# Kernel tuning notes

Hardware: AMD Instinct MI355X
Metric: run time of the kernel (lower is better)

The kernel has to match this reference:

```python
import jax, jax.numpy as jnp
import numpy as np

BN_EPS = 1e-5

def _conv(x, w, b, pad):
    # x: [B,C,H,W], w: [O,I,kh,kw] -> [B,O,H,W]
    y = jax.lax.conv_general_dilated(x, w, window_strides=(1, 1),
                                     padding=[(pad, pad), (pad, pad)],
                                     dimension_numbers=("NCHW", "OIHW", "NCHW"))
    return y + b[None, :, None, None]

def setup_inputs() -> dict:
    key = jax.random.key(0)
    ks = jax.random.split(key, 5)
    B, Cin, H, W = 2, 256, 80, 80
    Ck, Cv, Cout = 128, 256, 256
    std = 0.02  # matches torch normal_(0, 0.02) init
    return {
        "x": jax.random.normal(ks[0], (B, Cin, H, W), jnp.float32),
        "wk": std * jax.random.normal(ks[1], (Ck, Cin, 1, 1), jnp.float32),
        "bk": jnp.zeros((Ck,), jnp.float32),
        "gamma": jnp.ones((Ck,), jnp.float32),
        "beta": jnp.zeros((Ck,), jnp.float32),
        "rmean": jnp.zeros((Ck,), jnp.float32),
        "rvar": jnp.ones((Ck,), jnp.float32),
        "wv": std * jax.random.normal(ks[2], (Cv, Cin, 3, 3), jnp.float32),
        "bv": jnp.zeros((Cv,), jnp.float32),
        "ww": std * jax.random.normal(ks[3], (Cout, Cv, 1, 1), jnp.float32),
        "bw": jnp.zeros((Cout,), jnp.float32),
    }

def reference(x, wk, bk, gamma, beta, rmean, rvar, wv, bv, ww, bw):
    B, Cin, H, W = x.shape
    Ck, Cv = wk.shape[0], wv.shape[0]
    N = H * W

    # f_key == f_query (shared module): 1x1 conv + BatchNorm (inference stats)
    kq = _conv(x, wk, bk, pad=0)                      # [B,Ck,H,W]
    inv = gamma / jnp.sqrt(rvar + BN_EPS)
    kq = kq * inv[None, :, None, None] + (beta - rmean * inv)[None, :, None, None]
    kq = kq.reshape(B, Ck, N)                          # key layout [B,Ck,N]

    # f_value: 3x3 conv
    value = _conv(x, wv, bv, pad=1).reshape(B, Cv, N)  # [B,Cv,N]

    # sim_map = query^T @ key -> [B,N,N], full softmax over last dim
    sim = jnp.einsum("bcn,bcm->bnm", kq, kq)
    sim = jax.nn.softmax(sim, axis=-1)

    # context = sim @ value^T -> [B,N,Cv] -> [B,Cv,H,W]
    ctx = jnp.einsum("bnm,bcm->bcn", sim, value).reshape(B, Cv, H, W)

    out = _conv(ctx, ww, bw, pad=0) + x                # residual
    return out
```

## Files before the change

### kernel.cpp

```cpp
#include <hip/hip_runtime.h>
#include <math.h>

#define NB   2
#define CIN  256
#define IMH  80
#define IMW  80
#define NPIX (IMH*IMW)
#define CK   128
#define CVC  256
#define COUTC 256
#define BN_EPS 1e-5f
#define HP   82
#define WP   82
#define SPLIT 2
#define NC   (NPIX / SPLIT / 64)
#define NMC  (NPIX / 64)

typedef short sx8 __attribute__((ext_vector_type(8)));
typedef short sx4 __attribute__((ext_vector_type(4)));
typedef float f32x4 __attribute__((ext_vector_type(4)));

__device__ __forceinline__ short f2bf(float f) {
    unsigned u = __builtin_bit_cast(unsigned, f);
    u += 0x7fffu + ((u >> 16) & 1u);
    return (short)(u >> 16);
}
__device__ __forceinline__ float bf2f(short s) {
    unsigned u = ((unsigned)(unsigned short)s) << 16;
    return __builtin_bit_cast(float, u);
}

__global__ __launch_bounds__(256) void pad_kernel(const float* __restrict__ x,
                                                  short* __restrict__ xpad)
{
    __shared__ short T[64][258];
    const int tid = threadIdx.x;
    const int n0  = blockIdx.x * 64;
    const int b   = blockIdx.y;
    const float* xb = x + (size_t)b * CIN * NPIX;

    #pragma unroll 4
    for (int i = 0; i < 64; ++i) {
        int e = tid + i * 256;
        int pix = e & 63, c = e >> 6;
        T[pix][c] = f2bf(xb[(size_t)c * NPIX + n0 + pix]);
    }
    __syncthreads();
    #pragma unroll
    for (int i = 0; i < 8; ++i) {
        int e   = tid + i * 256;
        int pix = e >> 5;
        int cp  = (e & 31) * 8;
        int np  = n0 + pix;
        int hp  = np / IMW + 1, wp = np % IMW + 1;
        sx8 v = *(const sx8*)&T[pix][cp];
        *(sx8*)&xpad[(((size_t)b * HP + hp) * WP + wp) * CIN + cp] = v;
    }
}

__global__ __launch_bounds__(256) void wvt_kernel(const float* __restrict__ wv,
                                                  short* __restrict__ wvt)
{
    int idx = blockIdx.x * 256 + threadIdx.x;
    int tap = idx >> 16;
    int cv  = (idx >> 8) & 255;
    int c   = idx & 255;
    wvt[idx] = f2bf(wv[((size_t)cv * CIN + c) * 9 + tap]);
}

__global__ __launch_bounds__(256) void wwb_kernel(const float* __restrict__ ww,
                                                  short* __restrict__ wwb)
{
    int idx = blockIdx.x * 256 + threadIdx.x;
    wwb[idx] = f2bf(ww[idx]);
}

__global__ __launch_bounds__(256) void wkb_kernel(
    const float* __restrict__ wk, const float* __restrict__ bk,
    const float* __restrict__ gamma, const float* __restrict__ beta,
    const float* __restrict__ rmean, const float* __restrict__ rvar,
    short* __restrict__ wkb, float* __restrict__ bias2)
{
    int idx = blockIdx.x * 256 + threadIdx.x;
    int ck = idx >> 8;
    float inv = gamma[ck] * rsqrtf(rvar[ck] + BN_EPS);
    wkb[idx] = f2bf(wk[idx] * inv);
    if (idx < CK) {
        float invi = gamma[idx] * rsqrtf(rvar[idx] + BN_EPS);
        bias2[idx] = (bk[idx] - rmean[idx]) * invi + beta[idx];
    }
}

__global__ __launch_bounds__(256) void kq_kernel(
    const short* __restrict__ xpad, const short* __restrict__ wkb,
    const float* __restrict__ bias2, short* __restrict__ kqT)
{
    __shared__ short T[64][136];
    const int tid  = threadIdx.x;
    const int wid  = tid >> 6;
    const int lane = tid & 63;
    const int l15  = lane & 15;
    const int quad = lane >> 4;
    const int n0 = blockIdx.x * 64;
    const int b  = blockIdx.y;
    const short* xb = xpad + (size_t)b * HP * WP * CIN;
    const int ck0 = wid * 32;

    const short* brow[4];
    #pragma unroll
    for (int nt = 0; nt < 4; ++nt) {
        int n = n0 + nt * 16 + l15;
        int hp = n / IMW + 1, wp = n % IMW + 1;
        brow[nt] = xb + ((size_t)hp * WP + wp) * CIN;
    }

    f32x4 acc[2][4];
    #pragma unroll
    for (int at = 0; at < 2; ++at)
        #pragma unroll
        for (int nt = 0; nt < 4; ++nt)
            acc[at][nt] = (f32x4){0.f, 0.f, 0.f, 0.f};

    for (int kc = 0; kc < CIN / 32; ++kc) {
        sx8 af0 = *(const sx8*)&wkb[(size_t)(ck0 + l15) * CIN + kc * 32 + quad * 8];
        sx8 af1 = *(const sx8*)&wkb[(size_t)(ck0 + 16 + l15) * CIN + kc * 32 + quad * 8];
        #pragma unroll
        for (int nt = 0; nt < 4; ++nt) {
            sx8 bf = *(const sx8*)&brow[nt][kc * 32 + quad * 8];
            acc[0][nt] = __builtin_amdgcn_mfma_f32_16x16x32_bf16(af0, bf, acc[0][nt], 0, 0, 0);
            acc[1][nt] = __builtin_amdgcn_mfma_f32_16x16x32_bf16(af1, bf, acc[1][nt], 0, 0, 0);
        }
    }

    #pragma unroll
    for (int at = 0; at < 2; ++at) {
        f32x4 b4 = *(const f32x4*)&bias2[ck0 + at * 16 + quad * 4];
        #pragma unroll
        for (int nt = 0; nt < 4; ++nt)
            #pragma unroll
            for (int r = 0; r < 4; ++r)
                T[nt * 16 + l15][ck0 + at * 16 + quad * 4 + r] = f2bf(acc[at][nt][r] + b4[r]);
    }
    __syncthreads();
    #pragma unroll
    for (int it = 0; it < 4; ++it) {
        int e = tid + it * 256;
        int row = e >> 4, c8 = (e & 15) * 8;
        *(sx8*)&kqT[((size_t)b * NPIX + n0 + row) * CK + c8] = *(const sx8*)&T[row][c8];
    }
}

#define CSTRIDE 36
__global__ __launch_bounds__(256) void conv3_kernel(
    const short* __restrict__ xpad, const short* __restrict__ wvt,
    const float* __restrict__ bv, short* __restrict__ val)
{
    __shared__ __align__(16) short Xs[6 * 18 * CSTRIDE];

    const int tid  = threadIdx.x;
    const int wid  = tid >> 6;
    const int lane = tid & 63;
    const int l15  = lane & 15;
    const int quad = lane >> 4;

    const int rowT = blockIdx.x / 5, colT = blockIdx.x % 5;
    const int h0 = rowT * 4, w0 = colT * 16;
    const int cv0 = blockIdx.y * 64 + wid * 16;
    const int b   = blockIdx.z;

    const short* xb = xpad + (size_t)b * HP * WP * CIN;

    f32x4 acc[4];
    #pragma unroll
    for (int r = 0; r < 4; ++r) acc[r] = (f32x4){0.f, 0.f, 0.f, 0.f};

    for (int cc = 0; cc < CIN / 32; ++cc) {
        __syncthreads();
        #pragma unroll
        for (int i = 0; i < 2; ++i) {
            int e = tid + i * 256;
            if (e < 432) {
                int rc = e >> 2, l4 = e & 3;
                int row = rc / 18, col = rc % 18;
                sx8 v = *(const sx8*)&xb[(((size_t)(h0 + row)) * WP + (w0 + col)) * CIN + cc * 32 + l4 * 8];
                *(sx8*)&Xs[rc * CSTRIDE + l4 * 8] = v;
            }
        }
        __syncthreads();

        #pragma unroll
        for (int dw = 0; dw < 3; ++dw) {
            sx8 Bf[6];
            #pragma unroll
            for (int rr = 0; rr < 6; ++rr)
                Bf[rr] = *(const sx8*)&Xs[(rr * 18 + l15 + dw) * CSTRIDE + quad * 8];
            #pragma unroll
            for (int dh = 0; dh < 3; ++dh) {
                int tap = dh * 3 + dw;
                sx8 Af = *(const sx8*)&wvt[((size_t)(tap * 256 + cv0 + l15)) * CIN + cc * 32 + quad * 8];
                #pragma unroll
                for (int r = 0; r < 4; ++r)
                    acc[r] = __builtin_amdgcn_mfma_f32_16x16x32_bf16(Af, Bf[r + dh], acc[r], 0, 0, 0);
            }
        }
    }

    f32x4 bvv = *(const f32x4*)&bv[cv0 + quad * 4];
    #pragma unroll
    for (int r = 0; r < 4; ++r) {
        int n = (h0 + r) * IMW + w0 + l15;
        #pragma unroll
        for (int reg = 0; reg < 4; ++reg) {
            int cv = cv0 + quad * 4 + reg;
            val[((size_t)b * CVC + cv) * NPIX + n] = f2bf(acc[r][reg] + bvv[reg]);
        }
    }
}

__global__ __launch_bounds__(256) void repack_kernel(const short* __restrict__ val,
                                                     short* __restrict__ valF)
{
    const int tid = threadIdx.x;
    const int mc  = blockIdx.x;
    const int b   = blockIdx.y;
    const int mg  = tid & 7;
    const int cvb = tid >> 3;
    const int s2  = mg >> 2, qm = mg & 3;
    #pragma unroll
    for (int p = 0; p < 8; ++p) {
        int cv = cvb + p * 32;
        sx8 v = *(const sx8*)&val[((size_t)b * CVC + cv) * NPIX + mc * 64 + mg * 8];
        size_t d = ((((size_t)(b * NMC + mc) * 16 + (cv >> 4)) * 2 + s2) * 4 + qm) * 128
                 + (cv & 15) * 8;
        *(sx8*)&valF[d] = v;
    }
}

#define TQ 64
#define TK 64
#define KS_LD 136
#define PS_LD 66

__global__ __launch_bounds__(256) void attn_kernel(
    const short* __restrict__ kqT, const short* __restrict__ valF,
    short* __restrict__ opart, float* __restrict__ mpart, float* __restrict__ lpart)
{
    __shared__ __align__(16) short Ks[2][TK][KS_LD];
    __shared__ __align__(16) short Pb[2][TQ][PS_LD];
    __shared__ float arow[2][TQ];

    const int tid  = threadIdx.x;
    const int wid  = tid >> 6;
    const int lane = tid & 63;
    const int l15  = lane & 15;
    const int quad = lane >> 4;

    const int blk = blockIdx.x;
    const int b   = blk & 1;
    const int sp  = (blk >> 1) & 1;
    const int n0  = (blk >> 2) * TQ;
    const int mb  = sp * (NPIX / SPLIT);

    const short* kqb = kqT + (size_t)b * NPIX * CK;
    const short* vbase = valF + ((size_t)(b * NMC + sp * NC) * 16 + wid * 4) * 1024
                              + (size_t)lane * 8;

    const int srow = tid >> 4;
    const int sc8  = (tid & 15) * 8;

    sx8 qf[4];
    #pragma unroll
    for (int s = 0; s < 4; ++s)
        qf[s] = *(const sx8*)&kqb[(size_t)(n0 + wid * 16 + l15) * CK + s * 32 + quad * 8];

    sx8 kreg[4];
    #pragma unroll
    for (int p = 0; p < 4; ++p)
        kreg[p] = *(const sx8*)&kqb[(size_t)(mb + srow + p * 16) * CK + sc8];
    #pragma unroll
    for (int p = 0; p < 4; ++p)
        *(sx8*)&Ks[0][srow + p * 16][sc8] = kreg[p];

    sx8 vreg[8];
    #pragma unroll
    for (int s2 = 0; s2 < 2; ++s2)
        #pragma unroll
        for (int ct = 0; ct < 4; ++ct)
            vreg[s2 * 4 + ct] = *(const sx8*)&vbase[ct * 1024 + s2 * 512];

    float mq = -1e30f, lq = 0.f;
    f32x4 acc[4][4];
    #pragma unroll
    for (int qt = 0; qt < 4; ++qt)
        #pragma unroll
        for (int ct = 0; ct < 4; ++ct)
            acc[qt][ct] = (f32x4){0.f, 0.f, 0.f, 0.f};

    __syncthreads();

    for (int i = 0; i < NC; ++i) {
        const int cur = i & 1;
        const int m0  = mb + i * TK;

        if (i + 1 < NC) {
            #pragma unroll
            for (int p = 0; p < 4; ++p)
                kreg[p] = *(const sx8*)&kqb[(size_t)(m0 + TK + srow + p * 16) * CK + sc8];
        }

        f32x4 st[4];
        #pragma unroll
        for (int t2 = 0; t2 < 4; ++t2) st[t2] = (f32x4){0.f, 0.f, 0.f, 0.f};
        #pragma unroll
        for (int s = 0; s < 4; ++s) {
            #pragma unroll
            for (int t2 = 0; t2 < 4; ++t2) {
                sx8 af = *(const sx8*)&Ks[cur][t2 * 16 + l15][s * 32 + quad * 8];
                st[t2] = __builtin_amdgcn_mfma_f32_16x16x32_bf16(af, qf[s], st[t2], 0, 0, 0);
            }
        }

        float mx = st[0][0];
        #pragma unroll
        for (int t2 = 0; t2 < 4; ++t2)
            #pragma unroll
            for (int r = 0; r < 4; ++r)
                mx = fmaxf(mx, st[t2][r]);
        mx = fmaxf(mx, __shfl_xor(mx, 16));
        mx = fmaxf(mx, __shfl_xor(mx, 32));
        float mnew = fmaxf(mq, mx);
        float alpha = __expf(mq - mnew);
        mq = mnew;
        float sum = 0.f;
        #pragma unroll
        for (int t2 = 0; t2 < 4; ++t2) {
            #pragma unroll
            for (int r = 0; r < 4; ++r) {
                float p = __expf(st[t2][r] - mnew);
                st[t2][r] = p;
                sum += p;
            }
        }
        sum += __shfl_xor(sum, 16);
        sum += __shfl_xor(sum, 32);
        lq = lq * alpha + sum;

        if (quad == 0) arow[cur][wid * 16 + l15] = alpha;
        #pragma unroll
        for (int t2 = 0; t2 < 4; ++t2) {
            sx4 pw;
            #pragma unroll
            for (int r = 0; r < 4; ++r) pw[r] = f2bf(st[t2][r]);
            *(sx4*)&Pb[cur][wid * 16 + l15][t2 * 16 + quad * 4] = pw;
        }

        if (i + 1 < NC) {
            #pragma unroll
            for (int p = 0; p < 4; ++p)
                *(sx8*)&Ks[cur ^ 1][srow + p * 16][sc8] = kreg[p];
        }
        __syncthreads();

        #pragma unroll
        for (int qt = 0; qt < 4; ++qt) {
            f32x4 a4 = *(const f32x4*)&arow[cur][qt * 16 + quad * 4];
            #pragma unroll
            for (int ct = 0; ct < 4; ++ct)
                acc[qt][ct] *= a4;
        }
        #pragma unroll
        for (int s2 = 0; s2 < 2; ++s2) {
            sx8 pa[4];
            #pragma unroll
            for (int qt = 0; qt < 4; ++qt)
                pa[qt] = *(const sx8*)&Pb[cur][qt * 16 + l15][s2 * 32 + quad * 8];
            #pragma unroll
            for (int ct = 0; ct < 4; ++ct) {
                #pragma unroll
                for (int qt = 0; qt < 4; ++qt)
                    acc[qt][ct] = __builtin_amdgcn_mfma_f32_16x16x32_bf16(pa[qt], vreg[s2 * 4 + ct], acc[qt][ct], 0, 0, 0);
            }
        }

        if (i + 1 < NC) {
            #pragma unroll
            for (int s2 = 0; s2 < 2; ++s2)
                #pragma unroll
                for (int ct = 0; ct < 4; ++ct)
                    vreg[s2 * 4 + ct] = *(const sx8*)&vbase[(size_t)(i + 1) * 16384 + ct * 1024 + s2 * 512];
        }
    }

    size_t obase = (size_t)(sp * NB + b) * NPIX + n0;
    #pragma unroll
    for (int qt = 0; qt < 4; ++qt)
        #pragma unroll
        for (int ct = 0; ct < 4; ++ct) {
            int cv = wid * 64 + ct * 16 + l15;
            #pragma unroll
            for (int r = 0; r < 4; ++r)
                opart[(obase + qt * 16 + quad * 4 + r) * CVC + cv] = f2bf(acc[qt][ct][r]);
        }
    if (quad == 0) {
        mpart[obase + wid * 16 + l15] = mq;
        lpart[obase + wid * 16 + l15] = lq;
    }
}

#define BS_LD 40
__global__ __launch_bounds__(256) void out_kernel(
    const short* __restrict__ opart, const float* __restrict__ mpart,
    const float* __restrict__ lpart, const short* __restrict__ wwb,
    const float* __restrict__ bw, const float* __restrict__ x,
    float* __restrict__ out)
{
    __shared__ __align__(16) short Bs[64][BS_LD];
    __shared__ float w0s[64], w1s[64];

    const int tid  = threadIdx.x;
    const int wid  = tid >> 6;
    const int lane = tid & 63;
    const int l15  = lane & 15;
    const int quad = lane >> 4;

    const int n0  = blockIdx.x * 64;
    const int co0 = blockIdx.y * 64 + wid * 16;
    const int b   = blockIdx.z;

    if (tid < 64) {
        int n = n0 + tid;
        size_t r0 = (size_t)b * NPIX + n;
        size_t r1 = (size_t)(NB + b) * NPIX + n;
        float m0 = mpart[r0], m1 = mpart[r1];
        float l0 = lpart[r0], l1 = lpart[r1];
        float M  = fmaxf(m0, m1);
        float w0 = __expf(m0 - M), w1 = __expf(m1 - M);
        float rinv = 1.f / (w0 * l0 + w1 * l1);
        w0s[tid] = w0 * rinv;
        w1s[tid] = w1 * rinv;
    }

    const int srow = tid >> 2;
    const int sc8  = (tid & 3) * 8;
    const short* o0p = opart + ((size_t)b * NPIX + n0 + srow) * CVC + sc8;
    const short* o1p = o0p + (size_t)NB * NPIX * CVC;

    f32x4 acc[4];
    #pragma unroll
    for (int nt = 0; nt < 4; ++nt) acc[nt] = (f32x4){0.f, 0.f, 0.f, 0.f};

    for (int cc = 0; cc < CVC / 32; ++cc) {
        __syncthreads();
        {
            sx8 a = *(const sx8*)&o0p[cc * 32];
            sx8 bq = *(const sx8*)&o1p[cc * 32];
            float w0 = w0s[srow], w1 = w1s[srow];
            sx8 o;
            #pragma unroll
            for (int j = 0; j < 8; ++j)
                o[j] = f2bf(bf2f(a[j]) * w0 + bf2f(bq[j]) * w1);
            *(sx8*)&Bs[srow][sc8] = o;
        }
        __syncthreads();
        sx8 af = *(const sx8*)&wwb[(size_t)(co0 + l15) * CVC + cc * 32 + quad * 8];
        #pragma unroll
        for (int nt = 0; nt < 4; ++nt) {
            sx8 bf = *(const sx8*)&Bs[nt * 16 + l15][quad * 8];
            acc[nt] = __builtin_amdgcn_mfma_f32_16x16x32_bf16(af, bf, acc[nt], 0, 0, 0);
        }
    }

    f32x4 bv4 = *(const f32x4*)&bw[co0 + quad * 4];
    #pragma unroll
    for (int nt = 0; nt < 4; ++nt) {
        #pragma unroll
        for (int r = 0; r < 4; ++r) {
            int co = co0 + quad * 4 + r;
            int n  = n0 + nt * 16 + l15;
            size_t gi = ((size_t)b * COUTC + co) * NPIX + n;
            out[gi] = acc[nt][r] + bv4[r] + x[gi];
        }
    }
}

extern "C" void kernel_launch(void* const* d_in, const int* in_sizes, int n_in,
                              void* d_out, int out_size, void* d_ws, size_t ws_size,
                              hipStream_t stream)
{
    const float* x     = (const float*)d_in[0];
    const float* wk    = (const float*)d_in[1];
    const float* bk    = (const float*)d_in[2];
    const float* gamma = (const float*)d_in[3];
    const float* beta  = (const float*)d_in[4];
    const float* rmean = (const float*)d_in[5];
    const float* rvar  = (const float*)d_in[6];
    const float* wv    = (const float*)d_in[7];
    const float* bv    = (const float*)d_in[8];
    const float* ww    = (const float*)d_in[9];
    const float* bw    = (const float*)d_in[10];
    float* out = (float*)d_out;

    short* xpad  = (short*)d_ws;
    short* wvt   = xpad + (size_t)NB * HP * WP * CIN;
    short* vbuf  = wvt + (size_t)9 * CVC * CIN;
    short* opart = xpad;
    short* wwb   = vbuf + (size_t)NB * CVC * NPIX;
    short* wkb   = wwb  + (size_t)COUTC * CVC;
    short* kqT   = wkb  + (size_t)CK * CIN;
    short* valF  = kqT  + (size_t)NB * NPIX * CK;
    float* bias2 = (float*)(valF + (size_t)NB * NPIX * CVC);
    float* mpart = bias2 + CK;
    float* lpart = mpart + (size_t)SPLIT * NB * NPIX;

    hipMemsetAsync(xpad, 0, (size_t)NB * HP * WP * CIN * sizeof(short), stream);

    pad_kernel   <<<dim3(NPIX/64, NB),          256, 0, stream>>>(x, xpad);
    wvt_kernel   <<<(9*CVC*CIN)/256,            256, 0, stream>>>(wv, wvt);
    wwb_kernel   <<<(COUTC*CVC)/256,            256, 0, stream>>>(ww, wwb);
    wkb_kernel   <<<(CK*CIN)/256,               256, 0, stream>>>(wk, bk, gamma, beta, rmean, rvar, wkb, bias2);
    kq_kernel    <<<dim3(NPIX/64, NB),          256, 0, stream>>>(xpad, wkb, bias2, kqT);
    conv3_kernel <<<dim3(100, CVC/64,      NB), 256, 0, stream>>>(xpad, wvt, bv, vbuf);
    repack_kernel<<<dim3(NMC, NB),              256, 0, stream>>>(vbuf, valF);
    attn_kernel  <<<NB * SPLIT * (NPIX / TQ),   256, 0, stream>>>(kqT, valF, opart, mpart, lpart);
    out_kernel   <<<dim3(100, COUTC/64,    NB), 256, 0, stream>>>(opart, mpart, lpart, wwb, bw, x, out);
}
```

Measured before the change: 273.6 us.

## Load key fragments directly from global, drop LDS key staging, skip unit rescales

The attention kernel no longer stages key tiles through a double-buffered LDS array. Each lane now loads its MFMA key fragments straight from global memory (served by L1/L2), which removes the LDS stores, the register prefetch and one barrier's worth of traffic. The LDS saving is used to request three blocks per CU via launch bounds, and the P buffer row stride is widened. The accumulator rescale is skipped when every alpha in the wave equals one, removing redundant multiplies once the row max stabilizes. In exchange, key loads are exposed global latency with no explicit prefetch, and the tighter register budget may cause spills.

```diff
diff --git a/kernel.cpp b/kernel.cpp
--- a/kernel.cpp
+++ b/kernel.cpp
@@ -238,14 +238,12 @@
 
 #define TQ 64
 #define TK 64
-#define KS_LD 136
-#define PS_LD 66
-
-__global__ __launch_bounds__(256) void attn_kernel(
+#define PS_LD 72
+
+__global__ __launch_bounds__(256, 3) void attn_kernel(
     const short* __restrict__ kqT, const short* __restrict__ valF,
     short* __restrict__ opart, float* __restrict__ mpart, float* __restrict__ lpart)
 {
-    __shared__ __align__(16) short Ks[2][TK][KS_LD];
     __shared__ __align__(16) short Pb[2][TQ][PS_LD];
     __shared__ float arow[2][TQ];
 
@@ -264,23 +262,13 @@
     const short* kqb = kqT + (size_t)b * NPIX * CK;
     const short* vbase = valF + ((size_t)(b * NMC + sp * NC) * 16 + wid * 4) * 1024
                               + (size_t)lane * 8;
-
-    const int srow = tid >> 4;
-    const int sc8  = (tid & 15) * 8;
+    const short* kfb = kqb + (size_t)(mb + l15) * CK + quad * 8;
 
     sx8 qf[4];
     #pragma unroll
     for (int s = 0; s < 4; ++s)
         qf[s] = *(const sx8*)&kqb[(size_t)(n0 + wid * 16 + l15) * CK + s * 32 + quad * 8];
 
-    sx8 kreg[4];
-    #pragma unroll
-    for (int p = 0; p < 4; ++p)
-        kreg[p] = *(const sx8*)&kqb[(size_t)(mb + srow + p * 16) * CK + sc8];
-    #pragma unroll
-    for (int p = 0; p < 4; ++p)
-        *(sx8*)&Ks[0][srow + p * 16][sc8] = kreg[p];
-
     sx8 vreg[8];
     #pragma unroll
     for (int s2 = 0; s2 < 2; ++s2)
@@ -296,17 +284,9 @@
         for (int ct = 0; ct < 4; ++ct)
             acc[qt][ct] = (f32x4){0.f, 0.f, 0.f, 0.f};
 
-    __syncthreads();
-
     for (int i = 0; i < NC; ++i) {
         const int cur = i & 1;
-        const int m0  = mb + i * TK;
-
-        if (i + 1 < NC) {
-            #pragma unroll
-            for (int p = 0; p < 4; ++p)
-                kreg[p] = *(const sx8*)&kqb[(size_t)(m0 + TK + srow + p * 16) * CK + sc8];
-        }
+        const short* kf = kfb + (size_t)i * 64 * CK;
 
         f32x4 st[4];
         #pragma unroll
@@ -315,7 +295,7 @@
         for (int s = 0; s < 4; ++s) {
             #pragma unroll
             for (int t2 = 0; t2 < 4; ++t2) {
-                sx8 af = *(const sx8*)&Ks[cur][t2 * 16 + l15][s * 32 + quad * 8];
+                sx8 af = *(const sx8*)&kf[(size_t)(t2 * 16) * CK + s * 32];
                 st[t2] = __builtin_amdgcn_mfma_f32_16x16x32_bf16(af, qf[s], st[t2], 0, 0, 0);
             }
         }
@@ -353,20 +333,24 @@
             for (int r = 0; r < 4; ++r) pw[r] = f2bf(st[t2][r]);
             *(sx4*)&Pb[cur][wid * 16 + l15][t2 * 16 + quad * 4] = pw;
         }
-
-        if (i + 1 < NC) {
-            #pragma unroll
-            for (int p = 0; p < 4; ++p)
-                *(sx8*)&Ks[cur ^ 1][srow + p * 16][sc8] = kreg[p];
-        }
         __syncthreads();
 
-        #pragma unroll
-        for (int qt = 0; qt < 4; ++qt) {
-            f32x4 a4 = *(const f32x4*)&arow[cur][qt * 16 + quad * 4];
-            #pragma unroll
-            for (int ct = 0; ct < 4; ++ct)
-                acc[qt][ct] *= a4;
+        {
+            f32x4 a4[4];
+            #pragma unroll
+            for (int qt = 0; qt < 4; ++qt)
+                a4[qt] = *(const f32x4*)&arow[cur][qt * 16 + quad * 4];
+            float amin = fminf(fminf(a4[0][0], a4[0][1]), fminf(a4[0][2], a4[0][3]));
+            #pragma unroll
+            for (int qt = 1; qt < 4; ++qt)
+                amin = fminf(amin, fminf(fminf(a4[qt][0], a4[qt][1]), fminf(a4[qt][2], a4[qt][3])));
+            if (__any(amin < 1.0f)) {
+                #pragma unroll
+                for (int qt = 0; qt < 4; ++qt)
+                    #pragma unroll
+                    for (int ct = 0; ct < 4; ++ct)
+                        acc[qt][ct] *= a4[qt];
+            }
         }
         #pragma unroll
         for (int s2 = 0; s2 < 2; ++s2) {
```

Measured after the change: 398.2 us. 1.46x slower.
